# Optimization experiments

Hardware: AMD Instinct MI355X
Metric: run time of the kernel (lower is better)

Reference implementation:

```python
import jax, jax.numpy as jnp
import numpy as np

B, N, K, CIN, COUT, H = 4, 2048, 32, 16, 32, 32
EPS = 1e-5


def setup_inputs() -> dict:
    key = jax.random.key(0)
    ks = jax.random.split(key, 6)
    s = 0.1
    return dict(
        xyz=jax.random.uniform(ks[0], (B, N, 3), dtype=jnp.float32),
        points=jax.random.normal(ks[1], (B, N, CIN), dtype=jnp.float32),
        W1=jax.random.normal(ks[2], (3, H), dtype=jnp.float32) * s,
        b1=jnp.zeros((H,), jnp.float32),
        g1=jnp.ones((H,), jnp.float32),
        be1=jnp.zeros((H,), jnp.float32),
        W2=jax.random.normal(ks[3], (H, H), dtype=jnp.float32) * s,
        b2=jnp.zeros((H,), jnp.float32),
        g2=jnp.ones((H,), jnp.float32),
        be2=jnp.zeros((H,), jnp.float32),
        W3=jax.random.normal(ks[4], (H, CIN * COUT), dtype=jnp.float32) * s,
        b3=jnp.zeros((CIN * COUT,), jnp.float32),
        gbn=jnp.ones((COUT,), jnp.float32),
        bbn=jnp.zeros((COUT,), jnp.float32),
    )


def _bn(h, g, b):
    # BatchNorm1d training-mode math: biased batch stats over axis 0
    return g * (h - h.mean(0)) / jnp.sqrt(h.var(0) + EPS) + b


def reference(xyz, points, W1, b1, g1, be1, W2, b2, g2, be2, W3, b3, gbn, bbn):
    # KNN: squared distances (B,N,N)
    sq = jnp.sum(xyz * xyz, -1)
    dist = -2.0 * jnp.einsum('bmc,bnc->bmn', xyz, xyz) + sq[:, :, None] + sq[:, None, :]
    _, idx = jax.lax.top_k(-dist, K)  # (B,N,K) nearest neighbors

    gather = jax.vmap(lambda p, i: p[i])  # (N,C),(N,K)->(N,K,C), vmapped over B
    grouped_xyz = gather(xyz, idx)                      # (B,N,K,3)
    rel = grouped_xyz - xyz[:, :, None, :]              # (B,N,K,3)
    grouped_pts = gather(points, idx)                   # (B,N,K,CIN)

    # weight net on relative coords
    h = rel.reshape(-1, 3)
    h = _bn(jax.nn.relu(h @ W1 + b1), g1, be1)
    h = _bn(jax.nn.relu(h @ W2 + b2), g2, be2)
    w = (h @ W3 + b3).reshape(B, N, K, CIN, COUT)       # (B,N,K,CIN,COUT)

    # weighted sum over C_in, then max over neighbors
    out = jnp.einsum('bnkc,bnkco->bnko', grouped_pts, w)  # (B,N,K,COUT)
    out = out.max(axis=2)                                 # (B,N,COUT)

    # final BatchNorm1d over (B,N) per channel
    m = out.mean((0, 1))
    v = out.var((0, 1))
    return gbn * (out - m) / jnp.sqrt(v + EPS) + bbn
```

## Files before the change

### kernel.cpp

```cpp
#include <hip/hip_runtime.h>

#define B_ 4
#define N_ 2048
#define K_ 32
#define CIN_ 16
#define COUT_ 32
#define H_ 32
#define R_ (B_*N_*K_)
#define EPS_ 1e-5f
#define INVR_ (1.0f/(float)R_)
#define INVBN_ (1.0f/(float)(B_*N_))
#define LISTCAP 160
#define NSH 16

typedef __attribute__((ext_vector_type(8)))  _Float16 f16x8;
typedef __attribute__((ext_vector_type(2)))  __fp16   hw16x2;
typedef __attribute__((ext_vector_type(2)))  _Float16 f16x2;
typedef __attribute__((ext_vector_type(16))) float    f32x16;

__device__ __forceinline__ float dot3f(float ax,float ay,float az,float bx,float by,float bz){
    return fmaf(az,bz, fmaf(ay,by, ax*bx));
}
__device__ __forceinline__ unsigned int pk2(float a, float b){
    union { hw16x2 v; unsigned int u; } c;
    c.v = __builtin_amdgcn_cvt_pkrtz(a, b);
    return c.u;
}
__device__ __forceinline__ unsigned int pkmul(unsigned int a, unsigned int b){
    union { unsigned int u; f16x2 v; } x, y, r;
    x.u = a; y.u = b; r.v = x.v * y.v; return r.u;
}
__device__ __forceinline__ float shsum(const float* __restrict__ p, int k){
    float s = 0.f;
    #pragma unroll
    for (int i = 0; i < NSH; ++i) s += p[i*32 + k];
    return s;
}

__global__ __launch_bounds__(256) void k_prep0(const float* __restrict__ xyz, const float* __restrict__ points,
                                               float4* __restrict__ xs4g, unsigned int* __restrict__ pf16,
                                               float* __restrict__ st){
    int flat = blockIdx.x*256 + threadIdx.x;
    if (flat < 8192){
        float x = xyz[3*flat], y = xyz[3*flat+1], z = xyz[3*flat+2];
        xs4g[flat] = make_float4(x, y, z, dot3f(x,y,z,x,y,z));
    } else {
        int p = flat - 8192;
        pf16[p] = pk2(points[2*p], points[2*p+1]);
    }
    if (blockIdx.x == 0){
        for (int j = threadIdx.x; j < 3072; j += 256) st[j] = 0.f;
    }
}

__global__ __launch_bounds__(256,5) void k_knn(const float4* __restrict__ xs4g,
                                               const float* __restrict__ W1, const float* __restrict__ b1,
                                               int* __restrict__ idx_out,
                                               float* __restrict__ s1sh, float* __restrict__ q1sh,
                                               unsigned int* __restrict__ h1f){
    __shared__ unsigned int hist[4][512][2];
    __shared__ unsigned long long lst[4][LISTCAP];
    __shared__ int kidx[4][K_];

    const int tid  = threadIdx.x;
    const int w    = tid >> 6;
    const int lane = tid & 63;
    const int half = lane >> 5;
    const int b    = blockIdx.x >> 9;
    const int q    = ((blockIdx.x & 511) << 2) + w;
    const int bN   = b * N_;
    unsigned int* hw = &hist[w][0][0];

    const uint4 z4 = make_uint4(0,0,0,0);
    uint4* h4 = (uint4*)hw;
    #pragma unroll
    for (int i = 0; i < 4; ++i) h4[i*64 + lane] = z4;

    const float4 qp = xs4g[bN + q];
    const float qx = qp.x, qy = qp.y, qz = qp.z, sqq = qp.w;

    unsigned int fv[32];
    #pragma unroll
    for (int j = 0; j < 32; ++j){
        int c = j*64 + lane;
        float4 pt = xs4g[bN + c];
        float d = fmaf(-2.0f, dot3f(qx,qy,qz, pt.x,pt.y,pt.z), sqq) + pt.w;
        fv[j] = __float_as_uint(d);
        unsigned int u1 = __float_as_uint(d + 1.0f);
        unsigned int key = (u1 <= 0x3F800000u) ? 0u : ((u1 - 0x3F800000u) >> 15);
        key = key > 511u ? 511u : key;
        atomicAdd(&hw[key*2 + (lane & 1)], 1u);
    }

    unsigned int g[8];
    #pragma unroll
    for (int t = 0; t < 4; ++t){
        uint4 h = ((const uint4*)hw)[lane*4 + t];
        g[2*t]   = h.x + h.y;
        g[2*t+1] = h.z + h.w;
    }
    unsigned int gs = 0;
    #pragma unroll
    for (int t = 0; t < 8; ++t) gs += g[t];
    unsigned int cum = gs;
    #pragma unroll
    for (int off = 1; off < 64; off <<= 1){
        unsigned int v = __shfl_up(cum, off);
        if (lane >= off) cum += v;
    }
    unsigned long long bal = __ballot(cum >= (unsigned)K_);
    int L = __ffsll(bal) - 1;
    unsigned int run = __shfl(cum, L) - __shfl(gs, L);
    int Bsel = 8*L + 7;
    {
        unsigned int c = run; bool fnd = false;
        #pragma unroll
        for (int t = 0; t < 8; ++t){
            unsigned int ht = __shfl(g[t], L, 64);
            if (!fnd && c + ht >= (unsigned)K_){ Bsel = 8*L + t; fnd = true; }
            c += ht;
        }
    }
    const float Tedge = __uint_as_float(0x3F800000u + ((unsigned)(Bsel + 1) << 15));
    const bool allin = (Bsel == 511);

    const unsigned long long mlt = (lane == 63) ? ~0ull >> 1 : (1ull << lane) - 1ull;
    unsigned int cnt = 0;
    #pragma unroll
    for (int j = 0; j < 32; ++j){
        float f1 = __uint_as_float(fv[j]) + 1.0f;
        bool surv = (f1 < Tedge) || allin;
        unsigned long long sb = __ballot(surv);
        unsigned int pos = cnt + (unsigned int)__popcll(sb & mlt);
        if (surv && pos < (unsigned)LISTCAP)
            lst[w][pos] = ((unsigned long long)fv[j] << 32) | (unsigned int)(j*64 + lane);
        cnt += (unsigned int)__popcll(sb);
    }
    int m = (int)cnt; if (m > LISTCAP) m = LISTCAP;

    int* outp = idx_out + ((size_t)bN + q) * K_;
    for (int i = lane; i < m; i += 64){
        unsigned long long my = lst[w][i];
        int rank = 0;
        for (int jj = 0; jj < m; ++jj)
            rank += (lst[w][jj] < my) ? 1 : 0;
        if (rank < K_){
            int id = (int)(unsigned int)(my & 0xFFFFFFFFull);
            outp[rank] = id;
            kidx[w][rank] = id;
        }
    }

    {
        const int ch = lane & 31;
        float w1a = W1[ch], w1b = W1[H_+ch], w1c = W1[2*H_+ch], b1c = b1[ch];
        float s = 0.f, qq = 0.f;
        #pragma unroll
        for (int r = 0; r < 16; ++r){
            int idr = kidx[w][half*16 + r];
            float4 pn = xs4g[bN + idr];
            float rx = pn.x - qx, ry = pn.y - qy, rz = pn.z - qz;
            float h = fmaxf(fmaf(rx, w1a, fmaf(ry, w1b, fmaf(rz, w1c, b1c))), 0.0f);
            s += h; qq = fmaf(h, h, qq);
        }
        s  += __shfl_xor(s, 32, 64);
        qq += __shfl_xor(qq, 32, 64);
        if (lane < 32){
            int sh = (blockIdx.x & (NSH-1)) * 32 + ch;
            atomicAdd(&s1sh[sh], s);
            atomicAdd(&q1sh[sh], qq);
        }
    }

    {
        const int id = kidx[w][lane & 31];
        float4 pn = xs4g[bN + id];
        float rx = pn.x - qx, ry = pn.y - qy, rz = pn.z - qz;
        uint4* dst = (uint4*)h1f + (size_t)(bN + q)*128 + lane;
        const int c0 = half*8;
        #pragma unroll
        for (int sblk = 0; sblk < 2; ++sblk){
            const int cb = sblk*16 + c0;
            const float4 wa0 = *(const float4*)(W1 + cb);
            const float4 wa1 = *(const float4*)(W1 + cb + 4);
            const float4 wb0 = *(const float4*)(W1 + H_ + cb);
            const float4 wb1 = *(const float4*)(W1 + H_ + cb + 4);
            const float4 wc0 = *(const float4*)(W1 + 2*H_ + cb);
            const float4 wc1 = *(const float4*)(W1 + 2*H_ + cb + 4);
            const float4 bv0 = *(const float4*)(b1 + cb);
            const float4 bv1 = *(const float4*)(b1 + cb + 4);
            float h0 = fmaxf(fmaf(rx, wa0.x, fmaf(ry, wb0.x, fmaf(rz, wc0.x, bv0.x))), 0.0f);
            float h1v= fmaxf(fmaf(rx, wa0.y, fmaf(ry, wb0.y, fmaf(rz, wc0.y, bv0.y))), 0.0f);
            float h2v= fmaxf(fmaf(rx, wa0.z, fmaf(ry, wb0.z, fmaf(rz, wc0.z, bv0.z))), 0.0f);
            float h3 = fmaxf(fmaf(rx, wa0.w, fmaf(ry, wb0.w, fmaf(rz, wc0.w, bv0.w))), 0.0f);
            float h4 = fmaxf(fmaf(rx, wa1.x, fmaf(ry, wb1.x, fmaf(rz, wc1.x, bv1.x))), 0.0f);
            float h5 = fmaxf(fmaf(rx, wa1.y, fmaf(ry, wb1.y, fmaf(rz, wc1.y, bv1.y))), 0.0f);
            float h6 = fmaxf(fmaf(rx, wa1.z, fmaf(ry, wb1.z, fmaf(rz, wc1.z, bv1.z))), 0.0f);
            float h7 = fmaxf(fmaf(rx, wa1.w, fmaf(ry, wb1.w, fmaf(rz, wc1.w, bv1.w))), 0.0f);
            uint4 o;
            o.x = pk2(h0, h1v); o.y = pk2(h2v, h3); o.z = pk2(h4, h5); o.w = pk2(h6, h7);
            dst[sblk*64] = o;
        }
    }
}

__device__ __forceinline__ void build_l2(const float* __restrict__ s1s, const float* __restrict__ q1s,
                                         const float* __restrict__ g1, const float* __restrict__ be1,
                                         const float* __restrict__ W2, const float* __restrict__ b2,
                                         float* a1L, float* bb1L, unsigned int* W2L, float* b2pL,
                                         int tid){
    if (tid < H_){
        float s = shsum(s1s, tid), qq = shsum(q1s, tid);
        float mm = s*INVR_, vv = qq*INVR_ - mm*mm;
        float aa = g1[tid] / sqrtf(vv + EPS_);
        a1L[tid]  = aa;
        bb1L[tid] = fmaf(-aa, mm, be1[tid]);
    }
    __syncthreads();
    #pragma unroll
    for (int e = 0; e < 2; ++e){
        int d = tid*2 + e;
        int jj = d & 3, ln = (d >> 2) & 63, s = d >> 8;
        int col = ln & 31;
        int k0 = s*16 + ((ln >> 5) << 3) + 2*jj;
        W2L[d] = pk2(a1L[k0]*W2[k0*H_ + col], a1L[k0+1]*W2[(k0+1)*H_ + col]);
    }
    if (tid < H_){
        float acc = b2[tid];
        #pragma unroll 4
        for (int h = 0; h < H_; ++h) acc = fmaf(bb1L[h], W2[h*H_ + tid], acc);
        b2pL[tid] = acc;
    }
}

__global__ __launch_bounds__(256,4) void k_h2stats(const uint4* __restrict__ h1f,
                                                   const float* __restrict__ s1s, const float* __restrict__ q1s,
                                                   const float* __restrict__ g1, const float* __restrict__ be1,
                                                   const float* __restrict__ W2, const float* __restrict__ b2,
                                                   float* s2s, float* q2s){
    __shared__ float redS[H_], redQ[H_];
    __shared__ float a1L[H_], bb1L[H_], b2pL[H_];
    __shared__ unsigned int W2L[512];
    const int tid = threadIdx.x, lane = tid & 63, w = tid >> 6;
    const int m = lane & 31;
    if (tid < H_){ redS[tid] = 0.f; redQ[tid] = 0.f; }
    build_l2(s1s, q1s, g1, be1, W2, b2, a1L, bb1L, W2L, b2pL, tid);
    __syncthreads();

    union { uint4 u4; f16x8 v; } Bf0, Bf1;
    Bf0.u4 = ((const uint4*)W2L)[lane];
    Bf1.u4 = ((const uint4*)W2L)[64 + lane];
    float b2c = b2pL[m];
    const int blk0 = blockIdx.x*16 + w*4;

    float s = 0.f, q = 0.f;
    #pragma unroll
    for (int t = 0; t < 4; ++t){
        union { uint4 u4; f16x8 v; } a0, a1f;
        a0.u4  = h1f[(size_t)(blk0 + t)*128 + lane];
        a1f.u4 = h1f[(size_t)(blk0 + t)*128 + 64 + lane];
        f32x16 acc;
        #pragma unroll
        for (int i = 0; i < 16; ++i) acc[i] = b2c;
        acc = __builtin_amdgcn_mfma_f32_32x32x16_f16(a0.v,  Bf0.v, acc, 0, 0, 0);
        acc = __builtin_amdgcn_mfma_f32_32x32x16_f16(a1f.v, Bf1.v, acc, 0, 0, 0);
        #pragma unroll
        for (int i = 0; i < 16; ++i){
            float v = fmaxf(acc[i], 0.0f);
            s += v; q = fmaf(v, v, q);
        }
    }
    s += __shfl_xor(s, 32, 64);
    q += __shfl_xor(q, 32, 64);
    if (lane < 32){ atomicAdd(&redS[m], s); atomicAdd(&redQ[m], q); }
    __syncthreads();
    if (tid < H_){
        int sh = (blockIdx.x & (NSH-1)) * 32 + tid;
        atomicAdd(&s2s[sh], redS[tid]);
        atomicAdd(&q2s[sh], redQ[tid]);
    }
}

#define PHASEA(T, H2P, GSEL) do { \
    union { uint4 u4; f16x8 v; } B0f, B1f; \
    B0f.u4 = h1f[(size_t)(blk0 + (T))*128 + lane]; \
    B1f.u4 = h1f[(size_t)(blk0 + (T))*128 + 64 + lane]; \
    int row = rB + (T)*32 + m; \
    int bb_ = row >> 16; \
    int idr = idx[row]; \
    const uint4* gpp = (const uint4*)(pf16 + ((size_t)bb_*N_ + idr)*8); \
    uint4 ga = gpp[0], gb = gpp[1]; \
    GSEL[0] = half ? gb.x : ga.x; \
    GSEL[1] = half ? gb.y : ga.y; \
    GSEL[2] = half ? gb.z : ga.z; \
    GSEL[3] = half ? gb.w : ga.w; \
    f32x16 c2; \
    _Pragma("unroll") \
    for (int i = 0; i < 16; ++i) c2[i] = b2v[i]; \
    c2 = __builtin_amdgcn_mfma_f32_32x32x16_f16(A0.v, B0f.v, c2, 0, 0, 0); \
    c2 = __builtin_amdgcn_mfma_f32_32x32x16_f16(A1.v, B1f.v, c2, 0, 0, 0); \
    _Pragma("unroll") \
    for (int p = 0; p < 8; ++p){ \
        float v0 = fmaxf(c2[2*p],   0.0f); \
        float v1 = fmaxf(c2[2*p+1], 0.0f); \
        unsigned int ow = pk2(v0, v1); \
        unsigned int ot = __shfl_xor(ow, 32, 64); \
        int a = p >> 1, bb = p & 1; \
        H2P[4*a + bb]     = half ? ot : ow; \
        H2P[4*a + 2 + bb] = half ? ow : ot; \
    } \
} while(0)

#define REDST(ACC, T) do { \
    float v = ACC[0]; \
    _Pragma("unroll") \
    for (int i = 1; i < 16; ++i) v = fmaxf(v, ACC[i]); \
    v = fmaxf(v, __shfl_xor(v, 32, 64)); \
    if (lane < 32){ \
        int g = blk0 + (T); \
        out_pre[(size_t)g*COUT_ + m] = v; \
        atomicAdd(&redS[m], v); \
        atomicAdd(&redQ[m], v*v); \
    } \
} while(0)

__global__ __launch_bounds__(256,4) void k_out(const uint4* __restrict__ h1f, const int* __restrict__ idx,
                                               const float* __restrict__ s1s, const float* __restrict__ q1s,
                                               const float* __restrict__ g1, const float* __restrict__ be1,
                                               const float* __restrict__ W2, const float* __restrict__ b2,
                                               const float* __restrict__ s2s, const float* __restrict__ q2s,
                                               const float* __restrict__ g2, const float* __restrict__ be2,
                                               const float* __restrict__ W3, const float* __restrict__ b3,
                                               const unsigned int* __restrict__ pf16,
                                               float* __restrict__ out_pre, float* s3s, float* q3s){
    __shared__ uint4 Wls[2112];
    __shared__ float redS[COUT_], redQ[COUT_];
    __shared__ float a1L[H_], bb1L[H_], b2pL[H_], aa2L[H_], bb2L[H_];
    __shared__ unsigned int W2L[512];
    const int tid = threadIdx.x, lane = tid & 63, w = tid >> 6;
    const int half = lane >> 5, m = lane & 31;
    if (tid < COUT_){
        redS[tid] = 0.f; redQ[tid] = 0.f;
        float ss = shsum(s2s, tid), qq = shsum(q2s, tid);
        float mm = ss*INVR_, vv = qq*INVR_ - mm*mm;
        float aa = g2[tid] / sqrtf(vv + EPS_);
        aa2L[tid] = aa;
        bb2L[tid] = fmaf(-aa, mm, be2[tid]);
    }
    build_l2(s1s, q1s, g1, be1, W2, b2, a1L, bb1L, W2L, b2pL, tid);
    {
        int jj = tid & 3, ln = tid >> 2;
        int col = ln & 31, c0 = ((ln >> 5) << 3) + 2*jj;
        unsigned int* WlsD = (unsigned int*)Wls;
        #pragma unroll 4
        for (int i = 0; i < 32; ++i){
            float a = aa2L[i];
            WlsD[i*256 + tid] = pk2(a*W3[i*512 + c0*COUT_ + col], a*W3[i*512 + (c0+1)*COUT_ + col]);
        }
        float v0 = b3[c0*COUT_ + col], v1 = b3[(c0+1)*COUT_ + col];
        #pragma unroll 4
        for (int h = 0; h < H_; ++h){
            v0 = fmaf(bb2L[h], W3[h*512 + c0*COUT_ + col], v0);
            v1 = fmaf(bb2L[h], W3[h*512 + (c0+1)*COUT_ + col], v1);
        }
        WlsD[32*256 + tid] = pk2(v0, v1);
    }
    __syncthreads();

    const int rB = blockIdx.x*256 + w*64;
    const int blk0 = blockIdx.x*8 + w*2;

    union { uint4 u4; f16x8 v; } A0, A1;
    A0.u4 = ((const uint4*)W2L)[lane];
    A1.u4 = ((const uint4*)W2L)[64 + lane];
    float b2v[16];
    #pragma unroll
    for (int i = 0; i < 16; ++i) b2v[i] = b2pL[(i&3) + 8*(i>>2) + 4*half];

    unsigned int h2p0[16], h2p1[16];
    unsigned int gsel0[4], gsel1[4];
    PHASEA(0, h2p0, gsel0);
    PHASEA(1, h2p1, gsel1);

    f32x16 acc0, acc1;
    #pragma unroll
    for (int i = 0; i < 16; ++i){ acc0[i] = 0.f; acc1[i] = 0.f; }
    #pragma unroll
    for (int kb = 0; kb < 32; ++kb){
        union { uint4 u4; f16x8 v; } bf; bf.u4 = Wls[kb*64 + lane];
        const unsigned int sel = (kb & 1) ? 0x03020302u : 0x01000100u;
        unsigned int hr0 = h2p0[kb >> 1];
        unsigned int hd0 = __builtin_amdgcn_perm(hr0, hr0, sel);
        union { unsigned int u[4]; f16x8 v; } af;
        #pragma unroll
        for (int jj = 0; jj < 4; ++jj) af.u[jj] = pkmul(hd0, gsel0[jj]);
        acc0 = __builtin_amdgcn_mfma_f32_32x32x16_f16(af.v, bf.v, acc0, 0, 0, 0);
        unsigned int hr1 = h2p1[kb >> 1];
        unsigned int hd1 = __builtin_amdgcn_perm(hr1, hr1, sel);
        #pragma unroll
        for (int jj = 0; jj < 4; ++jj) af.u[jj] = pkmul(hd1, gsel1[jj]);
        acc1 = __builtin_amdgcn_mfma_f32_32x32x16_f16(af.v, bf.v, acc1, 0, 0, 0);
    }
    {
        union { uint4 u4; f16x8 v; } bf; bf.u4 = Wls[32*64 + lane];
        union { unsigned int u[4]; f16x8 v; } af;
        #pragma unroll
        for (int jj = 0; jj < 4; ++jj) af.u[jj] = gsel0[jj];
        acc0 = __builtin_amdgcn_mfma_f32_32x32x16_f16(af.v, bf.v, acc0, 0, 0, 0);
        #pragma unroll
        for (int jj = 0; jj < 4; ++jj) af.u[jj] = gsel1[jj];
        acc1 = __builtin_amdgcn_mfma_f32_32x32x16_f16(af.v, bf.v, acc1, 0, 0, 0);
    }

    REDST(acc0, 0);
    REDST(acc1, 1);

    __syncthreads();
    if (tid < COUT_){
        int sh = (blockIdx.x & (NSH-1)) * 32 + tid;
        atomicAdd(&s3s[sh], redS[tid]);
        atomicAdd(&q3s[sh], redQ[tid]);
    }
}

__global__ __launch_bounds__(256) void k_bn(const float4* __restrict__ out_pre4,
                                            const float* __restrict__ s3s, const float* __restrict__ q3s,
                                            const float* __restrict__ gbn, const float* __restrict__ bbn,
                                            float4* __restrict__ out4){
    __shared__ float aaL[COUT_], bbL[COUT_];
    const int tid = threadIdx.x;
    if (tid < COUT_){
        float ss = shsum(s3s, tid), qq = shsum(q3s, tid);
        float mm = ss*INVBN_, vv = qq*INVBN_ - mm*mm;
        float aa = gbn[tid]/sqrtf(vv + EPS_);
        aaL[tid] = aa;
        bbL[tid] = fmaf(-aa, mm, bbn[tid]);
    }
    __syncthreads();
    int i = blockIdx.x*256 + tid;
    int o = (i*4) & (COUT_-1);
    float4 v = out_pre4[i];
    float4 r;
    r.x = fmaf(aaL[o],   v.x, bbL[o]);
    r.y = fmaf(aaL[o+1], v.y, bbL[o+1]);
    r.z = fmaf(aaL[o+2], v.z, bbL[o+2]);
    r.w = fmaf(aaL[o+3], v.w, bbL[o+3]);
    out4[i] = r;
}

extern "C" void kernel_launch(void* const* d_in, const int* in_sizes, int n_in,
                              void* d_out, int out_size, void* d_ws, size_t ws_size,
                              hipStream_t stream){
    const float* xyz    = (const float*)d_in[0];
    const float* points = (const float*)d_in[1];
    const float* W1  = (const float*)d_in[2];
    const float* b1  = (const float*)d_in[3];
    const float* g1  = (const float*)d_in[4];
    const float* be1 = (const float*)d_in[5];
    const float* W2  = (const float*)d_in[6];
    const float* b2  = (const float*)d_in[7];
    const float* g2  = (const float*)d_in[8];
    const float* be2 = (const float*)d_in[9];
    const float* W3  = (const float*)d_in[10];
    const float* b3  = (const float*)d_in[11];
    const float* gbn = (const float*)d_in[12];
    const float* bbn = (const float*)d_in[13];
    float* out = (float*)d_out;

    char* base = (char*)d_ws;
    int*            idx     = (int*)(base + 0);
    float*          out_pre = (float*)(base + 1048576);
    unsigned int*   pf16    = (unsigned int*)(base + 2097152);
    float*          st      = (float*)(base + 2359296);
    float4*         xs4g    = (float4*)(base + 2371584);
    unsigned int*   h1f     = (unsigned int*)(base + 4194304);
    float *s1s=st, *q1s=st+512, *s2s=st+1024, *q2s=st+1536, *s3s=st+2048, *q3s=st+2560;

    hipLaunchKernelGGL(k_prep0,   dim3(288),      dim3(256), 0, stream, xyz, points, xs4g, pf16, st);
    hipLaunchKernelGGL(k_knn,     dim3(B_*N_/4),  dim3(256), 0, stream, xs4g, W1, b1, idx, s1s, q1s, h1f);
    hipLaunchKernelGGL(k_h2stats, dim3(R_/512),   dim3(256), 0, stream, (const uint4*)h1f,
                       s1s, q1s, g1, be1, W2, b2, s2s, q2s);
    hipLaunchKernelGGL(k_out,     dim3(R_/256),   dim3(256), 0, stream, (const uint4*)h1f, idx,
                       s1s, q1s, g1, be1, W2, b2, s2s, q2s, g2, be2, W3, b3, pf16, out_pre, s3s, q3s);
    hipLaunchKernelGGL(k_bn,      dim3(256),      dim3(256), 0, stream, (const float4*)out_pre, s3s, q3s,
                       gbn, bbn, (float4*)out);
}
```

Baseline: 161.1 us.

## Drop prep kernel; stage batch xyz in LDS inside KNN kernel

Removes the separate prep kernel. Each KNN block now loads its batch's xyz cloud into shared memory as SoA arrays and recomputes squared norms, instead of reading a precomputed float4 global buffer. The fp16 packing of points moves into the h2stats kernel, and stats zeroing becomes a memset. Each block redundantly loads 24KB of xyz and the extra shared memory lowers occupancy (launch bounds 5 to 3), in exchange for one fewer launch and LDS-speed neighbour reads.

Measured after the change: 155.1 us. -3.8%, faster.

```diff
diff --git a/kernel.cpp b/kernel.cpp
--- a/kernel.cpp
+++ b/kernel.cpp
@@ -37,27 +37,12 @@
     return s;
 }
 
-__global__ __launch_bounds__(256) void k_prep0(const float* __restrict__ xyz, const float* __restrict__ points,
-                                               float4* __restrict__ xs4g, unsigned int* __restrict__ pf16,
-                                               float* __restrict__ st){
-    int flat = blockIdx.x*256 + threadIdx.x;
-    if (flat < 8192){
-        float x = xyz[3*flat], y = xyz[3*flat+1], z = xyz[3*flat+2];
-        xs4g[flat] = make_float4(x, y, z, dot3f(x,y,z,x,y,z));
-    } else {
-        int p = flat - 8192;
-        pf16[p] = pk2(points[2*p], points[2*p+1]);
-    }
-    if (blockIdx.x == 0){
-        for (int j = threadIdx.x; j < 3072; j += 256) st[j] = 0.f;
-    }
-}
-
-__global__ __launch_bounds__(256,5) void k_knn(const float4* __restrict__ xs4g,
+__global__ __launch_bounds__(256,3) void k_knn(const float* __restrict__ xyz,
                                                const float* __restrict__ W1, const float* __restrict__ b1,
                                                int* __restrict__ idx_out,
                                                float* __restrict__ s1sh, float* __restrict__ q1sh,
                                                unsigned int* __restrict__ h1f){
+    __shared__ float sx[N_], sy[N_], sz[N_];
     __shared__ unsigned int hist[4][512][2];
     __shared__ unsigned long long lst[4][LISTCAP];
     __shared__ int kidx[4][K_];
@@ -71,20 +56,40 @@
     const int bN   = b * N_;
     unsigned int* hw = &hist[w][0][0];
 
+    {
+        const float4* xb4 = (const float4*)(xyz + (size_t)bN*3);
+        for (int k = tid; k < (N_*3)/4; k += 256){
+            float4 f = xb4[k];
+            int base = 4*k;
+            #pragma unroll
+            for (int j = 0; j < 4; ++j){
+                int g = base + j;
+                int pt = g/3, cp = g - pt*3;
+                float v = (j==0) ? f.x : (j==1) ? f.y : (j==2) ? f.z : f.w;
+                if (cp == 0) sx[pt] = v;
+                else if (cp == 1) sy[pt] = v;
+                else sz[pt] = v;
+            }
+        }
+    }
+
     const uint4 z4 = make_uint4(0,0,0,0);
     uint4* h4 = (uint4*)hw;
     #pragma unroll
     for (int i = 0; i < 4; ++i) h4[i*64 + lane] = z4;
 
-    const float4 qp = xs4g[bN + q];
-    const float qx = qp.x, qy = qp.y, qz = qp.z, sqq = qp.w;
+    __syncthreads();
+
+    const float qx = sx[q], qy = sy[q], qz = sz[q];
+    const float sqq = dot3f(qx,qy,qz,qx,qy,qz);
 
     unsigned int fv[32];
     #pragma unroll
     for (int j = 0; j < 32; ++j){
         int c = j*64 + lane;
-        float4 pt = xs4g[bN + c];
-        float d = fmaf(-2.0f, dot3f(qx,qy,qz, pt.x,pt.y,pt.z), sqq) + pt.w;
+        float px = sx[c], py = sy[c], pz = sz[c];
+        float pw = dot3f(px,py,pz,px,py,pz);
+        float d = fmaf(-2.0f, dot3f(qx,qy,qz,px,py,pz), sqq) + pw;
         fv[j] = __float_as_uint(d);
         unsigned int u1 = __float_as_uint(d + 1.0f);
         unsigned int key = (u1 <= 0x3F800000u) ? 0u : ((u1 - 0x3F800000u) >> 15);
@@ -158,8 +163,7 @@
         #pragma unroll
         for (int r = 0; r < 16; ++r){
             int idr = kidx[w][half*16 + r];
-            float4 pn = xs4g[bN + idr];
-            float rx = pn.x - qx, ry = pn.y - qy, rz = pn.z - qz;
+            float rx = sx[idr] - qx, ry = sy[idr] - qy, rz = sz[idr] - qz;
             float h = fmaxf(fmaf(rx, w1a, fmaf(ry, w1b, fmaf(rz, w1c, b1c))), 0.0f);
             s += h; qq = fmaf(h, h, qq);
         }
@@ -174,8 +178,7 @@
 
     {
         const int id = kidx[w][lane & 31];
-        float4 pn = xs4g[bN + id];
-        float rx = pn.x - qx, ry = pn.y - qy, rz = pn.z - qz;
+        float rx = sx[id] - qx, ry = sy[id] - qy, rz = sz[id] - qz;
         uint4* dst = (uint4*)h1f + (size_t)(bN + q)*128 + lane;
         const int c0 = half*8;
         #pragma unroll
@@ -234,6 +237,7 @@
 }
 
 __global__ __launch_bounds__(256,4) void k_h2stats(const uint4* __restrict__ h1f,
+                                                   const float* __restrict__ points, unsigned int* __restrict__ pf16,
                                                    const float* __restrict__ s1s, const float* __restrict__ q1s,
                                                    const float* __restrict__ g1, const float* __restrict__ be1,
                                                    const float* __restrict__ W2, const float* __restrict__ b2,
@@ -243,6 +247,10 @@
     __shared__ unsigned int W2L[512];
     const int tid = threadIdx.x, lane = tid & 63, w = tid >> 6;
     const int m = lane & 31;
+    {
+        int pp = blockIdx.x*256 + tid;
+        if (pp < 65536) pf16[pp] = pk2(points[2*pp], points[2*pp+1]);
+    }
     if (tid < H_){ redS[tid] = 0.f; redQ[tid] = 0.f; }
     build_l2(s1s, q1s, g1, be1, W2, b2, a1L, bb1L, W2L, b2pL, tid);
     __syncthreads();
@@ -472,14 +480,14 @@
     float*          out_pre = (float*)(base + 1048576);
     unsigned int*   pf16    = (unsigned int*)(base + 2097152);
     float*          st      = (float*)(base + 2359296);
-    float4*         xs4g    = (float4*)(base + 2371584);
     unsigned int*   h1f     = (unsigned int*)(base + 4194304);
     float *s1s=st, *q1s=st+512, *s2s=st+1024, *q2s=st+1536, *s3s=st+2048, *q3s=st+2560;
 
-    hipLaunchKernelGGL(k_prep0,   dim3(288),      dim3(256), 0, stream, xyz, points, xs4g, pf16, st);
-    hipLaunchKernelGGL(k_knn,     dim3(B_*N_/4),  dim3(256), 0, stream, xs4g, W1, b1, idx, s1s, q1s, h1f);
+    hipMemsetAsync((void*)st, 0, 12288, stream);
+
+    hipLaunchKernelGGL(k_knn,     dim3(B_*N_/4),  dim3(256), 0, stream, xyz, W1, b1, idx, s1s, q1s, h1f);
     hipLaunchKernelGGL(k_h2stats, dim3(R_/512),   dim3(256), 0, stream, (const uint4*)h1f,
-                       s1s, q1s, g1, be1, W2, b2, s2s, q2s);
+                       points, pf16, s1s, q1s, g1, be1, W2, b2, s2s, q2s);
     hipLaunchKernelGGL(k_out,     dim3(R_/256),   dim3(256), 0, stream, (const uint4*)h1f, idx,
                        s1s, q1s, g1, be1, W2, b2, s2s, q2s, g2, be2, W3, b3, pf16, out_pre, s3s, q3s);
     hipLaunchKernelGGL(k_bn,      dim3(256),      dim3(256), 0, stream, (const float4*)out_pre, s3s, q3s,
```
